# Kernel tuning notes

Hardware: AMD Instinct MI355X
Metric: run time of the kernel (lower is better)

Reference implementation:

```python
import jax, jax.numpy as jnp
import numpy as np

NUM_HEADS = 16
D_MODEL = 1024
HEAD_DIM = D_MODEL // NUM_HEADS
SCALE = 8.0 / HEAD_DIM  # use_mup=True
LN_EPS = 1e-5


def setup_inputs() -> dict:
    key = jax.random.key(0)
    ks = jax.random.split(key, 8)
    B, N, M = 2, 2048, 2048
    std = 1.0 / np.sqrt(D_MODEL)
    return {
        "x1": jax.random.normal(ks[0], (B, N, D_MODEL), jnp.float32),
        "x2": jax.random.normal(ks[1], (B, M, D_MODEL), jnp.float32),
        "Wq": jax.random.normal(ks[2], (D_MODEL, D_MODEL), jnp.float32) * std,
        "Wk": jax.random.normal(ks[3], (D_MODEL, D_MODEL), jnp.float32) * std,
        "Wv": jax.random.normal(ks[4], (D_MODEL, D_MODEL), jnp.float32) * std,
        "Wp": jax.random.normal(ks[5], (D_MODEL, D_MODEL), jnp.float32) * std,
        "bp": jnp.zeros((D_MODEL,), jnp.float32),
        "ln_g": jnp.ones((HEAD_DIM,), jnp.float32),
        "ln_b": jnp.zeros((HEAD_DIM,), jnp.float32),
    }


def _layernorm(x, g, b):
    # LayerNorm over last dim (head_dim), eps=1e-5, biased variance (torch default)
    mu = jnp.mean(x, axis=-1, keepdims=True)
    var = jnp.mean(jnp.square(x - mu), axis=-1, keepdims=True)
    return (x - mu) * jax.lax.rsqrt(var + LN_EPS) * g + b


def reference(x1, x2, Wq, Wk, Wv, Wp, bp, ln_g, ln_b):
    B, N, C = x1.shape
    M = x2.shape[1]
    H, D = NUM_HEADS, HEAD_DIM
    # torch Linear: y = x @ W.T  (no qkv bias); reshape to [B, H, L, D]
    q = (x1 @ Wq.T).reshape(B, N, H, D).transpose(0, 2, 1, 3)
    k = (x2 @ Wk.T).reshape(B, M, H, D).transpose(0, 2, 1, 3)
    v = (x2 @ Wv.T).reshape(B, M, H, D).transpose(0, 2, 1, 3)
    # per-head QK LayerNorm (shared params)
    q = _layernorm(q, ln_g, ln_b)
    k = _layernorm(k, ln_g, ln_b)
    q = q * SCALE
    attn = jnp.einsum("bhnd,bhmd->bhnm", q, k)
    attn = jax.nn.softmax(attn, axis=-1)  # causal=False, attn_drop=0
    out = jnp.einsum("bhnm,bhmd->bhnd", attn, v)
    out = out.transpose(0, 2, 1, 3).reshape(B, N, C)
    return out @ Wp.T + bp
```

## Files before the change

kernel.cpp:

```cpp
#include <hip/hip_runtime.h>

#define DEV static __device__ __forceinline__

using bf16x8 = __attribute__((ext_vector_type(8))) short;
using f32x4  = __attribute__((ext_vector_type(4))) float;
using f32x16 = __attribute__((ext_vector_type(16))) float;

#if __has_builtin(__builtin_amdgcn_exp2f)
#define EXP2(x) __builtin_amdgcn_exp2f(x)
#else
#define EXP2(x) exp2f(x)
#endif

DEV unsigned short f2bf(float f) {
  union { float f; unsigned u; } v; v.f = f;
  return (unsigned short)((v.u + 0x7fffu + ((v.u >> 16) & 1u)) >> 16);
}
DEV unsigned cvtpk(float lo, float hi) {
  unsigned r;
  asm("v_cvt_pk_bf16_f32 %0, %1, %2" : "=v"(r) : "v"(lo), "v"(hi));
  return r;
}
DEV void pl32swap(unsigned &a, unsigned &b) {
  asm("v_permlane32_swap_b32 %0, %1" : "+v"(a), "+v"(b));
}
DEV bf16x8 mk8(unsigned a, unsigned b, unsigned c, unsigned d) {
  union { unsigned u[4]; bf16x8 v; } t;
  t.u[0] = a; t.u[1] = b; t.u[2] = c; t.u[3] = d;
  return t.v;
}
DEV f32x4 mfma16(bf16x8 a, bf16x8 b, f32x4 c) {
  return __builtin_amdgcn_mfma_f32_16x16x32_bf16(a, b, c, 0, 0, 0);
}
DEV f32x16 mfma32(bf16x8 a, bf16x8 b, f32x16 c) {
  return __builtin_amdgcn_mfma_f32_32x32x16_bf16(a, b, c, 0, 0, 0);
}
DEV f32x16 zero16() {
  f32x16 z;
#pragma unroll
  for (int i = 0; i < 16; ++i) z[i] = 0.f;
  return z;
}

typedef const __attribute__((address_space(1))) unsigned int* gas1;
typedef __attribute__((address_space(3))) unsigned int* las3;
DEV void gl16(const void* g, void* l) {
  __builtin_amdgcn_global_load_lds((gas1)g, (las3)l, 16, 0, 0);
}

__global__ __launch_bounds__(256, 8)
void conv_bf16(const float* __restrict__ x1, const float* __restrict__ x2,
               const float* __restrict__ Wq, const float* __restrict__ Wk,
               const float* __restrict__ Wv, const float* __restrict__ Wp,
               unsigned short* __restrict__ o)
{
  size_t e = ((size_t)blockIdx.x * 256 + threadIdx.x) * 8;
  const float* s; size_t off;
  if (e < 4194304u)       { s = x1; off = e; }
  else if (e < 8388608u)  { s = x2; off = e - 4194304u; }
  else if (e < 9437184u)  { s = Wq; off = e - 8388608u; }
  else if (e < 10485760u) { s = Wk; off = e - 9437184u; }
  else if (e < 11534336u) { s = Wv; off = e - 10485760u; }
  else                    { s = Wp; off = e - 11534336u; }
  const float4* p = reinterpret_cast<const float4*>(s + off);
  float4 a = p[0], b = p[1];
  int4 r;
  r.x = (int)cvtpk(a.x, a.y); r.y = (int)cvtpk(a.z, a.w);
  r.z = (int)cvtpk(b.x, b.y); r.w = (int)cvtpk(b.z, b.w);
  *reinterpret_cast<int4*>(o + e) = r;
}

__global__ __launch_bounds__(256, 2)
void gemm_qkv_bf(const unsigned short* __restrict__ xb,
                 const float* __restrict__ lg, const float* __restrict__ lb,
                 unsigned short* __restrict__ qb, unsigned short* __restrict__ kb,
                 unsigned short* __restrict__ vtb)
{
  __shared__ short As[128 * 64];
  __shared__ short Bs[128 * 64];
  const int tid = threadIdx.x;
  const int l = tid & 63, w = tid >> 6;
  const int wr = w >> 1, wc = w & 1;
  const int z = blockIdx.z;
  const unsigned short* A = (z == 0) ? xb : (xb + 4194304);
  const unsigned short* W = xb + 8388608 + (size_t)z * 1048576;
  const int id = blockIdx.x + (blockIdx.y << 3);
  const int tl = ((id & 7) << 5) | (id >> 3);
  const int bx = tl & 7, by = tl >> 3;
  const int brow = by * 128, bcol = bx * 128;

  const f32x4 zero = {0.f, 0.f, 0.f, 0.f};
  f32x4 acc[4][4];
#pragma unroll
  for (int mi = 0; mi < 4; ++mi)
#pragma unroll
    for (int ni = 0; ni < 4; ++ni) acc[mi][ni] = zero;

  const int srow = w * 32 + (l >> 3);
  const int scol = (l & 7) * 8;

  for (int kt = 0; kt < 16; ++kt) {
    const unsigned short* ga = A + (size_t)(brow + srow) * 1024 + kt * 64 + scol;
    const unsigned short* gb = W + (size_t)(bcol + srow) * 1024 + kt * 64 + scol;
#pragma unroll
    for (int i = 0; i < 4; ++i) {
      gl16(ga + (size_t)i * 8 * 1024, &As[(w * 32 + i * 8) * 64]);
      gl16(gb + (size_t)i * 8 * 1024, &Bs[(w * 32 + i * 8) * 64]);
    }
    __syncthreads();
#pragma unroll
    for (int kk = 0; kk < 2; ++kk) {
      const int k0 = kk * 32 + ((l >> 4) << 3);
      bf16x8 af[4], bfr[4];
#pragma unroll
      for (int mi = 0; mi < 4; ++mi)
        af[mi] = *reinterpret_cast<const bf16x8*>(
            &As[((wr << 6) + (mi << 4) + (l & 15)) * 64 + k0]);
#pragma unroll
      for (int ni = 0; ni < 4; ++ni)
        bfr[ni] = *reinterpret_cast<const bf16x8*>(
            &Bs[((wc << 6) + (ni << 4) + (l & 15)) * 64 + k0]);
#pragma unroll
      for (int mi = 0; mi < 4; ++mi)
#pragma unroll
        for (int ni = 0; ni < 4; ++ni)
          acc[mi][ni] = mfma16(af[mi], bfr[ni], acc[mi][ni]);
    }
    __syncthreads();
  }

  if (z < 2) {
    unsigned short* dst = (z == 0) ? qb : kb;
    const float scl = (z == 0) ? 0.18033688011112042f : 1.0f;
    const int h = bx * 2 + wc;
    float gw4[4], bw4[4];
#pragma unroll
    for (int ni = 0; ni < 4; ++ni) {
      gw4[ni] = lg[ni * 16 + (l & 15)] * scl;
      bw4[ni] = lb[ni * 16 + (l & 15)] * scl;
    }
#pragma unroll
    for (int mi = 0; mi < 4; ++mi) {
      float ylo[4];
#pragma unroll
      for (int r = 0; r < 4; ++r) {
        float v0 = acc[mi][0][r], v1 = acc[mi][1][r];
        float v2 = acc[mi][2][r], v3 = acc[mi][3][r];
        float s  = (v0 + v1) + (v2 + v3);
        float s2 = (v0 * v0 + v1 * v1) + (v2 * v2 + v3 * v3);
#pragma unroll
        for (int off = 1; off < 16; off <<= 1) {
          s  += __shfl_xor(s, off);
          s2 += __shfl_xor(s2, off);
        }
        float mean = s * (1.f / 64.f);
        float var  = s2 * (1.f / 64.f) - mean * mean;
        float rstd = rsqrtf(var + 1e-5f);
        float y[4];
        y[0] = (v0 - mean) * rstd * gw4[0] + bw4[0];
        y[1] = (v1 - mean) * rstd * gw4[1] + bw4[1];
        y[2] = (v2 - mean) * rstd * gw4[2] + bw4[2];
        y[3] = (v3 - mean) * rstd * gw4[3] + bw4[3];
        if (!(r & 1)) {
          ylo[0] = y[0]; ylo[1] = y[1]; ylo[2] = y[2]; ylo[3] = y[3];
        } else {
          int rowg0 = brow + (wr << 6) + (mi << 4) + ((l >> 4) << 2) + r - 1;
          int b = rowg0 >> 11, n = rowg0 & 2047;
          unsigned short* base =
              dst + (((size_t)(b * 16 + h) << 11) + n) * 64 + (l & 15);
#pragma unroll
          for (int ni = 0; ni < 4; ++ni) {
            unsigned u = cvtpk(ylo[ni], y[ni]);
            base[ni * 16]      = (unsigned short)(u & 0xffffu);
            base[ni * 16 + 64] = (unsigned short)(u >> 16);
          }
        }
      }
    }
  } else {
    const int bb = brow >> 11;
    const int nblk = brow & 2047;
#pragma unroll
    for (int mi = 0; mi < 4; ++mi)
#pragma unroll
      for (int ni = 0; ni < 4; ++ni) {
        int n0 = nblk + (wr << 6) + (mi << 4) + ((l >> 4) << 2);
        int colg = bcol + (wc << 6) + (ni << 4) + (l & 15);
        int h = colg >> 6, d = colg & 63;
        unsigned u0 = cvtpk(acc[mi][ni][0], acc[mi][ni][1]);
        unsigned u1 = cvtpk(acc[mi][ni][2], acc[mi][ni][3]);
        int2 u; u.x = (int)u0; u.y = (int)u1;
        *reinterpret_cast<int2*>(
            &vtb[((size_t)(bb * 16 + h) * 64 + d) * 2048 + n0]) = u;
      }
  }
}

__global__ __launch_bounds__(128)
void attn_fwd(const unsigned short* __restrict__ Q,
              const unsigned short* __restrict__ K,
              const unsigned short* __restrict__ Vt,
              unsigned short* __restrict__ O)
{
  __shared__ short Ks[2][64 * 64];
  __shared__ short Vs[2][64 * 64];
  const int tid = threadIdx.x, w = tid >> 6, l = tid & 63;
  const int lo5 = l & 31, hi = l >> 5;
  const int bh = blockIdx.y;
  const int qbase = blockIdx.x * 64 + w * 32;
  const unsigned short* Qg = Q + ((size_t)bh * 2048 + qbase) * 64;
  const unsigned short* Kg = K + (size_t)bh * 2048 * 64;
  const unsigned short* Vg = Vt + (size_t)bh * 64 * 2048;

  bf16x8 qf[4];
#pragma unroll
  for (int ks = 0; ks < 4; ++ks)
    qf[ks] = *reinterpret_cast<const bf16x8*>(Qg + lo5 * 64 + ks * 16 + hi * 8);
  const bf16x8 ones = mk8(0x3F803F80u, 0x3F803F80u, 0x3F803F80u, 0x3F803F80u);

  f32x16 oc0 = zero16(), oc1 = zero16(), ls = zero16();

  const int srow = tid >> 3;
  const int sc8 = (tid & 7) * 8;
  const int swz = sc8 ^ ((srow & 7) << 3);

  int4 ka0, ka1, ka2, ka3, va0, va1, va2, va3;
  ka0 = *reinterpret_cast<const int4*>(Kg + (srow)      * 64 + sc8);
  ka1 = *reinterpret_cast<const int4*>(Kg + (srow + 16) * 64 + sc8);
  ka2 = *reinterpret_cast<const int4*>(Kg + (srow + 32) * 64 + sc8);
  ka3 = *reinterpret_cast<const int4*>(Kg + (srow + 48) * 64 + sc8);
  va0 = *reinterpret_cast<const int4*>(Vg + (size_t)(srow)      * 2048 + sc8);
  va1 = *reinterpret_cast<const int4*>(Vg + (size_t)(srow + 16) * 2048 + sc8);
  va2 = *reinterpret_cast<const int4*>(Vg + (size_t)(srow + 32) * 2048 + sc8);
  va3 = *reinterpret_cast<const int4*>(Vg + (size_t)(srow + 48) * 2048 + sc8);
  *reinterpret_cast<int4*>(&Ks[0][((srow)      << 6) + swz]) = ka0;
  *reinterpret_cast<int4*>(&Ks[0][((srow + 16) << 6) + swz]) = ka1;
  *reinterpret_cast<int4*>(&Ks[0][((srow + 32) << 6) + swz]) = ka2;
  *reinterpret_cast<int4*>(&Ks[0][((srow + 48) << 6) + swz]) = ka3;
  *reinterpret_cast<int4*>(&Vs[0][((srow)      << 6) + swz]) = va0;
  *reinterpret_cast<int4*>(&Vs[0][((srow + 16) << 6) + swz]) = va1;
  *reinterpret_cast<int4*>(&Vs[0][((srow + 32) << 6) + swz]) = va2;
  *reinterpret_cast<int4*>(&Vs[0][((srow + 48) << 6) + swz]) = va3;
  __syncthreads();

  const unsigned short* kp = Kg + 4096 + srow * 64 + sc8;
  const unsigned short* vp = Vg + 64 + (size_t)srow * 2048 + sc8;

  for (int it = 0; it < 32; ++it) {
    const int cur = it & 1;
    const short* Kc = Ks[cur];
    const short* Vc = Vs[cur];

    if (it < 31) {
      ka0 = *reinterpret_cast<const int4*>(kp);
      ka1 = *reinterpret_cast<const int4*>(kp + 1024);
      ka2 = *reinterpret_cast<const int4*>(kp + 2048);
      ka3 = *reinterpret_cast<const int4*>(kp + 3072);
      va0 = *reinterpret_cast<const int4*>(vp);
      va1 = *reinterpret_cast<const int4*>(vp + 32768);
      va2 = *reinterpret_cast<const int4*>(vp + 65536);
      va3 = *reinterpret_cast<const int4*>(vp + 98304);
      kp += 4096; vp += 64;
    }

    f32x16 s0 = zero16(), s1 = zero16();
    __builtin_amdgcn_s_setprio(1);
#pragma unroll
    for (int ks = 0; ks < 4; ++ks) {
      const int colc = (16 * ks + 8 * hi) ^ ((lo5 & 7) << 3);
      bf16x8 k0 = *reinterpret_cast<const bf16x8*>(&Kc[(lo5 << 6) + colc]);
      s0 = mfma32(k0, qf[ks], s0);
      bf16x8 k1 = *reinterpret_cast<const bf16x8*>(&Kc[((32 + lo5) << 6) + colc]);
      s1 = mfma32(k1, qf[ks], s1);
    }
    __builtin_amdgcn_s_setprio(0);

    auto pvsub = [&](const f32x16& sv, int jbase) {
      float p0[16];
#pragma unroll
      for (int r = 0; r < 16; ++r) p0[r] = EXP2(sv[r]);
#pragma unroll
      for (int f = 0; f < 2; ++f) {
        unsigned x  = cvtpk(p0[8 * f + 0], p0[8 * f + 1]);
        unsigned zz = cvtpk(p0[8 * f + 2], p0[8 * f + 3]);
        unsigned y  = cvtpk(p0[8 * f + 4], p0[8 * f + 5]);
        unsigned ww = cvtpk(p0[8 * f + 6], p0[8 * f + 7]);
        pl32swap(x, y);
        pl32swap(zz, ww);
        bf16x8 pa = mk8(x, zz, y, ww);
        const int colc = (jbase + 16 * f + 8 * hi);
        bf16x8 v0 = *reinterpret_cast<const bf16x8*>(
            &Vc[(lo5 << 6) + (colc ^ ((lo5 & 7) << 3))]);
        bf16x8 v1 = *reinterpret_cast<const bf16x8*>(
            &Vc[((32 + lo5) << 6) + (colc ^ ((lo5 & 7) << 3))]);
        __builtin_amdgcn_s_setprio(1);
        oc0 = mfma32(pa, v0, oc0);
        oc1 = mfma32(pa, v1, oc1);
        ls  = mfma32(pa, ones, ls);
        __builtin_amdgcn_s_setprio(0);
      }
    };
    pvsub(s0, 0);
    pvsub(s1, 32);

    if (it < 31) {
      const int nb = cur ^ 1;
      *reinterpret_cast<int4*>(&Ks[nb][((srow)      << 6) + swz]) = ka0;
      *reinterpret_cast<int4*>(&Ks[nb][((srow + 16) << 6) + swz]) = ka1;
      *reinterpret_cast<int4*>(&Ks[nb][((srow + 32) << 6) + swz]) = ka2;
      *reinterpret_cast<int4*>(&Ks[nb][((srow + 48) << 6) + swz]) = ka3;
      *reinterpret_cast<int4*>(&Vs[nb][((srow)      << 6) + swz]) = va0;
      *reinterpret_cast<int4*>(&Vs[nb][((srow + 16) << 6) + swz]) = va1;
      *reinterpret_cast<int4*>(&Vs[nb][((srow + 32) << 6) + swz]) = va2;
      *reinterpret_cast<int4*>(&Vs[nb][((srow + 48) << 6) + swz]) = va3;
    }
    __syncthreads();
  }

  unsigned short* Og = O + ((size_t)(bh >> 4) * 2048 + qbase) * 1024 + (bh & 15) * 64;
#pragma unroll
  for (int r = 0; r < 16; ++r) {
    int qrow = (r & 3) + 8 * (r >> 2) + 4 * hi;
    float ir = __builtin_amdgcn_rcpf(ls[r]);
    Og[qrow * 1024 + lo5]      = f2bf(oc0[r] * ir);
    Og[qrow * 1024 + 32 + lo5] = f2bf(oc1[r] * ir);
  }
}

__global__ __launch_bounds__(256, 2)
void gemm_out_bf(const unsigned short* __restrict__ ob,
                 const unsigned short* __restrict__ wpb,
                 const float* __restrict__ bp, float* __restrict__ out)
{
  __shared__ short As[128 * 64];
  __shared__ short Bs[128 * 64];
  const int tid = threadIdx.x;
  const int l = tid & 63, w = tid >> 6;
  const int wr = w >> 1, wc = w & 1;
  const int id = blockIdx.x + (blockIdx.y << 3);
  const int tl = ((id & 7) << 5) | (id >> 3);
  const int brow = (tl >> 3) * 128, bcol = (tl & 7) * 128;

  const f32x4 zero = {0.f, 0.f, 0.f, 0.f};
  f32x4 acc[4][4];
#pragma unroll
  for (int mi = 0; mi < 4; ++mi)
#pragma unroll
    for (int ni = 0; ni < 4; ++ni) acc[mi][ni] = zero;

  const int srow = w * 32 + (l >> 3);
  const int scol = (l & 7) * 8;

  for (int kt = 0; kt < 16; ++kt) {
    const unsigned short* ga = ob + (size_t)(brow + srow) * 1024 + kt * 64 + scol;
    const unsigned short* gb = wpb + (size_t)(bcol + srow) * 1024 + kt * 64 + scol;
#pragma unroll
    for (int i = 0; i < 4; ++i) {
      gl16(ga + (size_t)i * 8 * 1024, &As[(w * 32 + i * 8) * 64]);
      gl16(gb + (size_t)i * 8 * 1024, &Bs[(w * 32 + i * 8) * 64]);
    }
    __syncthreads();
#pragma unroll
    for (int kk = 0; kk < 2; ++kk) {
      const int k0 = kk * 32 + ((l >> 4) << 3);
      bf16x8 af[4], bfr[4];
#pragma unroll
      for (int mi = 0; mi < 4; ++mi)
        af[mi] = *reinterpret_cast<const bf16x8*>(
            &As[((wr << 6) + (mi << 4) + (l & 15)) * 64 + k0]);
#pragma unroll
      for (int ni = 0; ni < 4; ++ni)
        bfr[ni] = *reinterpret_cast<const bf16x8*>(
            &Bs[((wc << 6) + (ni << 4) + (l & 15)) * 64 + k0]);
#pragma unroll
      for (int mi = 0; mi < 4; ++mi)
#pragma unroll
        for (int ni = 0; ni < 4; ++ni)
          acc[mi][ni] = mfma16(af[mi], bfr[ni], acc[mi][ni]);
    }
    __syncthreads();
  }

  float bias[4];
#pragma unroll
  for (int ni = 0; ni < 4; ++ni)
    bias[ni] = bp[bcol + (wc << 6) + (ni << 4) + (l & 15)];
#pragma unroll
  for (int mi = 0; mi < 4; ++mi)
#pragma unroll
    for (int ni = 0; ni < 4; ++ni)
#pragma unroll
      for (int r = 0; r < 4; ++r) {
        int rowg = brow + (wr << 6) + (mi << 4) + ((l >> 4) << 2) + r;
        int colg = bcol + (wc << 6) + (ni << 4) + (l & 15);
        out[(size_t)rowg * 1024 + colg] = acc[mi][ni][r] + bias[ni];
      }
}

extern "C" void kernel_launch(void* const* d_in, const int* in_sizes, int n_in,
                              void* d_out, int out_size, void* d_ws, size_t ws_size,
                              hipStream_t stream)
{
  const float* x1 = (const float*)d_in[0];
  const float* x2 = (const float*)d_in[1];
  const float* Wq = (const float*)d_in[2];
  const float* Wk = (const float*)d_in[3];
  const float* Wv = (const float*)d_in[4];
  const float* Wp = (const float*)d_in[5];
  const float* bp = (const float*)d_in[6];
  const float* lg = (const float*)d_in[7];
  const float* lb = (const float*)d_in[8];

  char* wsb = (char*)d_ws;
  unsigned short* xb   = (unsigned short*)wsb;
  unsigned short* qb   = (unsigned short*)(wsb + 25165824);
  unsigned short* kb   = qb + 4194304;
  unsigned short* vtb  = kb + 4194304;
  unsigned short* obuf = vtb + 4194304;
  float* out = (float*)d_out;

  conv_bf16<<<6144, 256, 0, stream>>>(x1, x2, Wq, Wk, Wv, Wp, xb);
  gemm_qkv_bf<<<dim3(8, 32, 3), 256, 0, stream>>>(xb, lg, lb, qb, kb, vtb);
  attn_fwd<<<dim3(32, 32), 128, 0, stream>>>(qb, kb, vtb, obuf);
  gemm_out_bf<<<dim3(8, 32), 256, 0, stream>>>(obuf,
      xb + 11534336, bp, out);
}
```

Before: 130.7 us.

## Fuse K and V projections into one GEMM sharing the x2 tile

The K and V projections now run in a single block: the x2 A-tile is loaded once into shared memory and multiplied against both Wk and Wv tiles, using a second accumulator set. The grid drops from three z-slices to two, so Q blocks do one GEMM while K/V blocks do two. This removes the duplicate A loads for V but doubles accumulator registers and adds a third shared buffer, which may reduce occupancy and unbalance work between the Q and K/V blocks.

```diff
diff --git a/kernel.cpp b/kernel.cpp
--- a/kernel.cpp
+++ b/kernel.cpp
@@ -78,35 +78,43 @@
 {
   __shared__ short As[128 * 64];
   __shared__ short Bs[128 * 64];
+  __shared__ short Cs[128 * 64];
   const int tid = threadIdx.x;
   const int l = tid & 63, w = tid >> 6;
   const int wr = w >> 1, wc = w & 1;
   const int z = blockIdx.z;
-  const unsigned short* A = (z == 0) ? xb : (xb + 4194304);
-  const unsigned short* W = xb + 8388608 + (size_t)z * 1048576;
+  const unsigned short* A  = (z == 0) ? xb : (xb + 4194304);
+  const unsigned short* W1 = xb + 8388608 + (z ? 1048576 : 0);
+  const unsigned short* W2 = xb + 10485760;
   const int id = blockIdx.x + (blockIdx.y << 3);
   const int tl = ((id & 7) << 5) | (id >> 3);
   const int bx = tl & 7, by = tl >> 3;
   const int brow = by * 128, bcol = bx * 128;
 
   const f32x4 zero = {0.f, 0.f, 0.f, 0.f};
-  f32x4 acc[4][4];
+  f32x4 acc[4][4], acc2[4][4];
 #pragma unroll
   for (int mi = 0; mi < 4; ++mi)
 #pragma unroll
-    for (int ni = 0; ni < 4; ++ni) acc[mi][ni] = zero;
+    for (int ni = 0; ni < 4; ++ni) { acc[mi][ni] = zero; acc2[mi][ni] = zero; }
 
   const int srow = w * 32 + (l >> 3);
   const int scol = (l & 7) * 8;
 
   for (int kt = 0; kt < 16; ++kt) {
-    const unsigned short* ga = A + (size_t)(brow + srow) * 1024 + kt * 64 + scol;
-    const unsigned short* gb = W + (size_t)(bcol + srow) * 1024 + kt * 64 + scol;
+    const unsigned short* ga = A  + (size_t)(brow + srow) * 1024 + kt * 64 + scol;
+    const unsigned short* gb = W1 + (size_t)(bcol + srow) * 1024 + kt * 64 + scol;
 #pragma unroll
     for (int i = 0; i < 4; ++i) {
       gl16(ga + (size_t)i * 8 * 1024, &As[(w * 32 + i * 8) * 64]);
       gl16(gb + (size_t)i * 8 * 1024, &Bs[(w * 32 + i * 8) * 64]);
     }
+    if (z) {
+      const unsigned short* gc = W2 + (size_t)(bcol + srow) * 1024 + kt * 64 + scol;
+#pragma unroll
+      for (int i = 0; i < 4; ++i)
+        gl16(gc + (size_t)i * 8 * 1024, &Cs[(w * 32 + i * 8) * 64]);
+    }
     __syncthreads();
 #pragma unroll
     for (int kk = 0; kk < 2; ++kk) {
@@ -125,11 +133,23 @@
 #pragma unroll
         for (int ni = 0; ni < 4; ++ni)
           acc[mi][ni] = mfma16(af[mi], bfr[ni], acc[mi][ni]);
+      if (z) {
+        bf16x8 cfr[4];
+#pragma unroll
+        for (int ni = 0; ni < 4; ++ni)
+          cfr[ni] = *reinterpret_cast<const bf16x8*>(
+              &Cs[((wc << 6) + (ni << 4) + (l & 15)) * 64 + k0]);
+#pragma unroll
+        for (int mi = 0; mi < 4; ++mi)
+#pragma unroll
+          for (int ni = 0; ni < 4; ++ni)
+            acc2[mi][ni] = mfma16(af[mi], cfr[ni], acc2[mi][ni]);
+      }
     }
     __syncthreads();
   }
 
-  if (z < 2) {
+  {
     unsigned short* dst = (z == 0) ? qb : kb;
     const float scl = (z == 0) ? 0.18033688011112042f : 1.0f;
     const int h = bx * 2 + wc;
@@ -177,7 +197,8 @@
         }
       }
     }
-  } else {
+  }
+  if (z) {
     const int bb = brow >> 11;
     const int nblk = brow & 2047;
 #pragma unroll
@@ -187,8 +208,8 @@
         int n0 = nblk + (wr << 6) + (mi << 4) + ((l >> 4) << 2);
         int colg = bcol + (wc << 6) + (ni << 4) + (l & 15);
         int h = colg >> 6, d = colg & 63;
-        unsigned u0 = cvtpk(acc[mi][ni][0], acc[mi][ni][1]);
-        unsigned u1 = cvtpk(acc[mi][ni][2], acc[mi][ni][3]);
+        unsigned u0 = cvtpk(acc2[mi][ni][0], acc2[mi][ni][1]);
+        unsigned u1 = cvtpk(acc2[mi][ni][2], acc2[mi][ni][3]);
         int2 u; u.x = (int)u0; u.y = (int)u1;
         *reinterpret_cast<int2*>(
             &vtb[((size_t)(bb * 16 + h) * 64 + d) * 2048 + n0]) = u;
@@ -420,7 +441,7 @@
   float* out = (float*)d_out;
 
   conv_bf16<<<6144, 256, 0, stream>>>(x1, x2, Wq, Wk, Wv, Wp, xb);
-  gemm_qkv_bf<<<dim3(8, 32, 3), 256, 0, stream>>>(xb, lg, lb, qb, kb, vtb);
+  gemm_qkv_bf<<<dim3(8, 32, 2), 256, 0, stream>>>(xb, lg, lb, qb, kb, vtb);
   attn_fwd<<<dim3(32, 32), 128, 0, stream>>>(qb, kb, vtb, obuf);
   gemm_out_bf<<<dim3(8, 32), 256, 0, stream>>>(obuf,
       xb + 11534336, bp, out);
```

Result: slower. 134.8 us (+3.1%).

## Process 64 query rows per wave in attention to reuse K/V fragments

Applied to the files above, without the earlier changes.

Each attention wave now handles two 32-row query sub-tiles instead of one, so every K and V fragment read from LDS feeds two MFMAs. The block covers 128 queries and the grid in x is halved to 16. The aim is to cut LDS traffic and global K/V loads per query. The cost is about double the accumulator registers and half as many blocks (512 on 256 CUs), which lowers occupancy and latency hiding.

```diff
diff --git a/kernel.cpp b/kernel.cpp
--- a/kernel.cpp
+++ b/kernel.cpp
@@ -196,7 +196,7 @@
   }
 }
 
-__global__ __launch_bounds__(128)
+__global__ __launch_bounds__(128, 1)
 void attn_fwd(const unsigned short* __restrict__ Q,
               const unsigned short* __restrict__ K,
               const unsigned short* __restrict__ Vt,
@@ -207,18 +207,21 @@
   const int tid = threadIdx.x, w = tid >> 6, l = tid & 63;
   const int lo5 = l & 31, hi = l >> 5;
   const int bh = blockIdx.y;
-  const int qbase = blockIdx.x * 64 + w * 32;
+  const int qbase = blockIdx.x * 128 + w * 64;
   const unsigned short* Qg = Q + ((size_t)bh * 2048 + qbase) * 64;
   const unsigned short* Kg = K + (size_t)bh * 2048 * 64;
   const unsigned short* Vg = Vt + (size_t)bh * 64 * 2048;
 
-  bf16x8 qf[4];
-#pragma unroll
-  for (int ks = 0; ks < 4; ++ks)
-    qf[ks] = *reinterpret_cast<const bf16x8*>(Qg + lo5 * 64 + ks * 16 + hi * 8);
+  bf16x8 qfA[4], qfB[4];
+#pragma unroll
+  for (int ks = 0; ks < 4; ++ks) {
+    qfA[ks] = *reinterpret_cast<const bf16x8*>(Qg + lo5 * 64 + ks * 16 + hi * 8);
+    qfB[ks] = *reinterpret_cast<const bf16x8*>(Qg + (32 + lo5) * 64 + ks * 16 + hi * 8);
+  }
   const bf16x8 ones = mk8(0x3F803F80u, 0x3F803F80u, 0x3F803F80u, 0x3F803F80u);
 
-  f32x16 oc0 = zero16(), oc1 = zero16(), ls = zero16();
+  f32x16 oc0a = zero16(), oc1a = zero16(), lsa = zero16();
+  f32x16 oc0b = zero16(), oc1b = zero16(), lsb = zero16();
 
   const int srow = tid >> 3;
   const int sc8 = (tid & 7) * 8;
@@ -263,45 +266,57 @@
       kp += 4096; vp += 64;
     }
 
-    f32x16 s0 = zero16(), s1 = zero16();
+    f32x16 s0a = zero16(), s1a = zero16(), s0b = zero16(), s1b = zero16();
     __builtin_amdgcn_s_setprio(1);
 #pragma unroll
     for (int ks = 0; ks < 4; ++ks) {
       const int colc = (16 * ks + 8 * hi) ^ ((lo5 & 7) << 3);
       bf16x8 k0 = *reinterpret_cast<const bf16x8*>(&Kc[(lo5 << 6) + colc]);
-      s0 = mfma32(k0, qf[ks], s0);
       bf16x8 k1 = *reinterpret_cast<const bf16x8*>(&Kc[((32 + lo5) << 6) + colc]);
-      s1 = mfma32(k1, qf[ks], s1);
+      s0a = mfma32(k0, qfA[ks], s0a);
+      s1a = mfma32(k1, qfA[ks], s1a);
+      s0b = mfma32(k0, qfB[ks], s0b);
+      s1b = mfma32(k1, qfB[ks], s1b);
     }
     __builtin_amdgcn_s_setprio(0);
 
-    auto pvsub = [&](const f32x16& sv, int jbase) {
-      float p0[16];
-#pragma unroll
-      for (int r = 0; r < 16; ++r) p0[r] = EXP2(sv[r]);
+    auto pvpair = [&](const f32x16& sa, const f32x16& sb, int jbase) {
+      float pA[16], pB[16];
+#pragma unroll
+      for (int r = 0; r < 16; ++r) { pA[r] = EXP2(sa[r]); pB[r] = EXP2(sb[r]); }
 #pragma unroll
       for (int f = 0; f < 2; ++f) {
-        unsigned x  = cvtpk(p0[8 * f + 0], p0[8 * f + 1]);
-        unsigned zz = cvtpk(p0[8 * f + 2], p0[8 * f + 3]);
-        unsigned y  = cvtpk(p0[8 * f + 4], p0[8 * f + 5]);
-        unsigned ww = cvtpk(p0[8 * f + 6], p0[8 * f + 7]);
-        pl32swap(x, y);
-        pl32swap(zz, ww);
-        bf16x8 pa = mk8(x, zz, y, ww);
+        unsigned xA  = cvtpk(pA[8 * f + 0], pA[8 * f + 1]);
+        unsigned zA  = cvtpk(pA[8 * f + 2], pA[8 * f + 3]);
+        unsigned yA  = cvtpk(pA[8 * f + 4], pA[8 * f + 5]);
+        unsigned wA  = cvtpk(pA[8 * f + 6], pA[8 * f + 7]);
+        pl32swap(xA, yA);
+        pl32swap(zA, wA);
+        bf16x8 paA = mk8(xA, zA, yA, wA);
+        unsigned xB  = cvtpk(pB[8 * f + 0], pB[8 * f + 1]);
+        unsigned zB  = cvtpk(pB[8 * f + 2], pB[8 * f + 3]);
+        unsigned yB  = cvtpk(pB[8 * f + 4], pB[8 * f + 5]);
+        unsigned wB  = cvtpk(pB[8 * f + 6], pB[8 * f + 7]);
+        pl32swap(xB, yB);
+        pl32swap(zB, wB);
+        bf16x8 paB = mk8(xB, zB, yB, wB);
         const int colc = (jbase + 16 * f + 8 * hi);
         bf16x8 v0 = *reinterpret_cast<const bf16x8*>(
             &Vc[(lo5 << 6) + (colc ^ ((lo5 & 7) << 3))]);
         bf16x8 v1 = *reinterpret_cast<const bf16x8*>(
             &Vc[((32 + lo5) << 6) + (colc ^ ((lo5 & 7) << 3))]);
         __builtin_amdgcn_s_setprio(1);
-        oc0 = mfma32(pa, v0, oc0);
-        oc1 = mfma32(pa, v1, oc1);
-        ls  = mfma32(pa, ones, ls);
+        oc0a = mfma32(paA, v0, oc0a);
+        oc1a = mfma32(paA, v1, oc1a);
+        lsa  = mfma32(paA, ones, lsa);
+        oc0b = mfma32(paB, v0, oc0b);
+        oc1b = mfma32(paB, v1, oc1b);
+        lsb  = mfma32(paB, ones, lsb);
         __builtin_amdgcn_s_setprio(0);
       }
     };
-    pvsub(s0, 0);
-    pvsub(s1, 32);
+    pvpair(s0a, s0b, 0);
+    pvpair(s1a, s1b, 32);
 
     if (it < 31) {
       const int nb = cur ^ 1;
@@ -321,9 +336,12 @@
 #pragma unroll
   for (int r = 0; r < 16; ++r) {
     int qrow = (r & 3) + 8 * (r >> 2) + 4 * hi;
-    float ir = __builtin_amdgcn_rcpf(ls[r]);
-    Og[qrow * 1024 + lo5]      = f2bf(oc0[r] * ir);
-    Og[qrow * 1024 + 32 + lo5] = f2bf(oc1[r] * ir);
+    float ira = __builtin_amdgcn_rcpf(lsa[r]);
+    Og[qrow * 1024 + lo5]      = f2bf(oc0a[r] * ira);
+    Og[qrow * 1024 + 32 + lo5] = f2bf(oc1a[r] * ira);
+    float irb = __builtin_amdgcn_rcpf(lsb[r]);
+    Og[(32 + qrow) * 1024 + lo5]      = f2bf(oc0b[r] * irb);
+    Og[(32 + qrow) * 1024 + 32 + lo5] = f2bf(oc1b[r] * irb);
   }
 }
 
@@ -421,7 +439,7 @@
 
   conv_bf16<<<6144, 256, 0, stream>>>(x1, x2, Wq, Wk, Wv, Wp, xb);
   gemm_qkv_bf<<<dim3(8, 32, 3), 256, 0, stream>>>(xb, lg, lb, qb, kb, vtb);
-  attn_fwd<<<dim3(32, 32), 128, 0, stream>>>(qb, kb, vtb, obuf);
+  attn_fwd<<<dim3(16, 32), 128, 0, stream>>>(qb, kb, vtb, obuf);
   gemm_out_bf<<<dim3(8, 32), 256, 0, stream>>>(obuf,
       xb + 11534336, bp, out);
 }
```

Result: no change. 129.4 us (-1.0%).
